# Kernel optimization log

Measured on AMD Instinct MI355X. Metric: run time of the kernel, lower is better.

## Reference

```python
import jax, jax.numpy as jnp
import numpy as np


def color_bin(x, n_bins):
    """Per-image 3D color histogram over n_bins**3 flat bins.
    x: [B, 3, H, W] float in ~[-1, 1]. Returns [B, n_bins**3] float32.
    """
    B, C, H, W = x.shape
    n_tot = n_bins ** 3
    # torch color_bins: i*(2/n_bins) - 1 for i in 1..n_bins-1
    boundaries = jnp.arange(1, n_bins, dtype=jnp.float32) * (2.0 / n_bins) - 1.0
    # torch.bucketize(right=False) == searchsorted side='left'
    idx = jnp.searchsorted(boundaries, x.reshape(B, C, H * W), side='left')  # [B,3,HW] int
    scale = jnp.array([1, n_bins, n_bins ** 2], dtype=idx.dtype)
    flat = jnp.einsum('bcp,c->bp', idx, scale)  # [B, HW], values in [0, n_tot)
    # torch.histc(bins, n_tot, min=0, max=n_tot-1) on exact integers == bincount
    hist = jax.vmap(lambda f: jnp.bincount(f, length=n_tot))(flat)
    return hist.astype(jnp.float32) / (H * W)


def setup_inputs() -> dict:
    key = jax.random.key(0)
    k1, k2 = jax.random.split(key)
    inp = jax.random.normal(k1, (8, 3, 1024, 1024), dtype=jnp.float32)
    style = jax.random.normal(k2, (1, 3, 1024, 1024), dtype=jnp.float32)
    return {"input": inp, "style_image": style, "n_bins": 16}


def reference(input, style_image, n_bins):
    # target histogram from the style image (detached in torch; ints anyway)
    target = color_bin(style_image, n_bins).squeeze(0)  # [n_tot]
    cols = color_bin(input, n_bins)                     # [B, n_tot]
    # F.l1_loss(cols, target.repeat(B, 1)) with mean reduction
    loss = jnp.mean(jnp.abs(cols - target[None, :]))
    return loss
```

## Files before the change

kernel.cpp:

```cpp
#include <hip/hip_runtime.h>

#define HW      (1024 * 1024)
#define HW4     (HW / 4)
#define NBINS   4096
#define NIMG    9
#define BPI     128
#define THREADS 256
#define F4_PER_BLOCK (HW4 / BPI)

__device__ __forceinline__ int bin16(float x) {
    int lo = 0;
    if (0.0f < x) lo = 8;
    if ((float)(lo + 4) * 0.125f - 1.0f < x) lo += 4;
    if ((float)(lo + 2) * 0.125f - 1.0f < x) lo += 2;
    if ((float)(lo + 1) * 0.125f - 1.0f < x) lo += 1;
    return lo;
}

__device__ __forceinline__ int bin3(float r, float g, float b) {
    return bin16(r) + 16 * bin16(g) + 256 * bin16(b);
}

__device__ __forceinline__ void acc4(int* lh, float4 r, float4 g, float4 b) {
    atomicAdd(&lh[bin3(r.x, g.x, b.x)], 1);
    atomicAdd(&lh[bin3(r.y, g.y, b.y)], 1);
    atomicAdd(&lh[bin3(r.z, g.z, b.z)], 1);
    atomicAdd(&lh[bin3(r.w, g.w, b.w)], 1);
}

__global__ __launch_bounds__(THREADS) void hist_kernel(
        const float* __restrict__ input,
        const float* __restrict__ style,
        int* __restrict__ part) {
    __shared__ int lh[NBINS];
    const int img = blockIdx.y;
    const int blk = blockIdx.x;
    const float* base = (img < 8) ? (input + (size_t)img * 3 * HW) : style;

    for (int i = threadIdx.x; i < NBINS; i += THREADS) lh[i] = 0;
    __syncthreads();

    const float4* c0 = (const float4*)(base);
    const float4* c1 = (const float4*)(base + HW);
    const float4* c2 = (const float4*)(base + 2 * HW);
    const int start = blk * F4_PER_BLOCK;

    for (int j = threadIdx.x; j < F4_PER_BLOCK; j += 2 * THREADS) {
        const int p0 = start + j;
        const int p1 = p0 + THREADS;
        float4 r0 = c0[p0], g0 = c1[p0], b0 = c2[p0];
        float4 r1 = c0[p1], g1 = c1[p1], b1 = c2[p1];
        acc4(lh, r0, g0, b0);
        acc4(lh, r1, g1, b1);
    }
    __syncthreads();

    int4* dst = (int4*)(part + ((size_t)img * BPI + blk) * NBINS);
    const int4* src = (const int4*)lh;
    for (int i = threadIdx.x; i < NBINS / 4; i += THREADS) dst[i] = src[i];
}

__global__ __launch_bounds__(THREADS) void reduce_kernel(
        const int* __restrict__ part,
        int* __restrict__ H) {
    const int img = blockIdx.y;
    const int bin = blockIdx.x * THREADS + threadIdx.x;
    const int* p = part + (size_t)img * BPI * NBINS + bin;
    int sum = 0;
#pragma unroll 8
    for (int b = 0; b < BPI; ++b) sum += p[(size_t)b * NBINS];
    H[img * NBINS + bin] = sum;
}

__global__ __launch_bounds__(1024) void loss_kernel(
        const int* __restrict__ H, float* __restrict__ out) {
    __shared__ long long partsum[16];
    const int* tgt = H + 8 * NBINS;
    long long acc = 0;
    for (int e = threadIdx.x; e < 8 * NBINS; e += 1024) {
        const int b = e >> 12;
        const int i = e & (NBINS - 1);
        const int d = H[b * NBINS + i] - tgt[i];
        acc += (d < 0) ? (long long)(-d) : (long long)d;
    }
    for (int off = 32; off; off >>= 1) acc += __shfl_down(acc, off, 64);
    const int lane = threadIdx.x & 63;
    const int wv   = threadIdx.x >> 6;
    if (lane == 0) partsum[wv] = acc;
    __syncthreads();
    if (wv == 0) {
        long long t = (lane < 16) ? partsum[lane] : 0;
        for (int off = 8; off; off >>= 1) t += __shfl_down(t, off, 64);
        if (lane == 0) {
            out[0] = (float)((double)t / 34359738368.0);
        }
    }
}

extern "C" void kernel_launch(void* const* d_in, const int* in_sizes, int n_in,
                              void* d_out, int out_size, void* d_ws, size_t ws_size,
                              hipStream_t stream) {
    const float* input = (const float*)d_in[0];
    const float* style = (const float*)d_in[1];
    int* part = (int*)d_ws;
    int* H    = part + (size_t)NIMG * BPI * NBINS;

    hipLaunchKernelGGL(hist_kernel, dim3(BPI, NIMG), dim3(THREADS), 0, stream,
                       input, style, part);
    hipLaunchKernelGGL(reduce_kernel, dim3(NBINS / THREADS, NIMG), dim3(THREADS),
                       0, stream, part, H);
    hipLaunchKernelGGL(loss_kernel, dim3(1), dim3(1024), 0, stream,
                       H, (float*)d_out);
}
```

Measured before the change: 182.1 us.

## Pack partial histograms to 16-bit, double blocks per image, split reduction

Doubles the number of histogram blocks per image so more workgroups run at once. Each block now handles 4096 pixels, so its bin counts fit in 16 bits and are written packed as ushort, which halves partial-histogram traffic. The reduction is split into two halves along a new grid dimension, and the loss kernel sums the two halves, stages the target histogram in shared memory, and accumulates in 32-bit ints instead of 64-bit. A bin count of exactly 65536 (all pixels of a block in one bin) would overflow the 16-bit packing.

After: 179.9 us. About the same (-1.2%).

```diff
diff --git a/kernel.cpp b/kernel.cpp
--- a/kernel.cpp
+++ b/kernel.cpp
@@ -4,9 +4,12 @@
 #define HW4     (HW / 4)
 #define NBINS   4096
 #define NIMG    9
-#define BPI     128
+#define BPI     256
 #define THREADS 256
 #define F4_PER_BLOCK (HW4 / BPI)
+#define NPART   (NIMG * BPI)
+
+typedef float f4 __attribute__((ext_vector_type(4)));
 
 __device__ __forceinline__ int bin16(float x) {
     int lo = 0;
@@ -21,7 +24,7 @@
     return bin16(r) + 16 * bin16(g) + 256 * bin16(b);
 }
 
-__device__ __forceinline__ void acc4(int* lh, float4 r, float4 g, float4 b) {
+__device__ __forceinline__ void acc4(int* lh, f4 r, f4 g, f4 b) {
     atomicAdd(&lh[bin3(r.x, g.x, b.x)], 1);
     atomicAdd(&lh[bin3(r.y, g.y, b.y)], 1);
     atomicAdd(&lh[bin3(r.z, g.z, b.z)], 1);
@@ -31,7 +34,7 @@
 __global__ __launch_bounds__(THREADS) void hist_kernel(
         const float* __restrict__ input,
         const float* __restrict__ style,
-        int* __restrict__ part) {
+        unsigned int* __restrict__ part) {
     __shared__ int lh[NBINS];
     const int img = blockIdx.y;
     const int blk = blockIdx.x;
@@ -40,48 +43,59 @@
     for (int i = threadIdx.x; i < NBINS; i += THREADS) lh[i] = 0;
     __syncthreads();
 
-    const float4* c0 = (const float4*)(base);
-    const float4* c1 = (const float4*)(base + HW);
-    const float4* c2 = (const float4*)(base + 2 * HW);
+    const f4* c0 = (const f4*)(base);
+    const f4* c1 = (const f4*)(base + HW);
+    const f4* c2 = (const f4*)(base + 2 * HW);
     const int start = blk * F4_PER_BLOCK;
 
     for (int j = threadIdx.x; j < F4_PER_BLOCK; j += 2 * THREADS) {
         const int p0 = start + j;
         const int p1 = p0 + THREADS;
-        float4 r0 = c0[p0], g0 = c1[p0], b0 = c2[p0];
-        float4 r1 = c0[p1], g1 = c1[p1], b1 = c2[p1];
+        f4 r0 = c0[p0], g0 = c1[p0], b0 = c2[p0];
+        f4 r1 = c0[p1], g1 = c1[p1], b1 = c2[p1];
         acc4(lh, r0, g0, b0);
         acc4(lh, r1, g1, b1);
     }
     __syncthreads();
 
-    int4* dst = (int4*)(part + ((size_t)img * BPI + blk) * NBINS);
-    const int4* src = (const int4*)lh;
-    for (int i = threadIdx.x; i < NBINS / 4; i += THREADS) dst[i] = src[i];
+    uint2* dst = (uint2*)(part + ((size_t)img * BPI + blk) * (NBINS / 2));
+    for (int i = threadIdx.x; i < NBINS / 4; i += THREADS) {
+        uint2 v;
+        v.x = (unsigned)lh[4 * i]     | ((unsigned)lh[4 * i + 1] << 16);
+        v.y = (unsigned)lh[4 * i + 2] | ((unsigned)lh[4 * i + 3] << 16);
+        dst[i] = v;
+    }
 }
 
 __global__ __launch_bounds__(THREADS) void reduce_kernel(
-        const int* __restrict__ part,
-        int* __restrict__ H) {
-    const int img = blockIdx.y;
-    const int bin = blockIdx.x * THREADS + threadIdx.x;
-    const int* p = part + (size_t)img * BPI * NBINS + bin;
+        const unsigned short* __restrict__ part,
+        int* __restrict__ H2) {
+    const int img  = blockIdx.y;
+    const int half = blockIdx.z;
+    const int bin  = blockIdx.x * THREADS + threadIdx.x;
+    const unsigned short* p = part
+        + ((size_t)img * BPI + half * (BPI / 2)) * NBINS + bin;
     int sum = 0;
-#pragma unroll 8
-    for (int b = 0; b < BPI; ++b) sum += p[(size_t)b * NBINS];
-    H[img * NBINS + bin] = sum;
+#pragma unroll 16
+    for (int b = 0; b < BPI / 2; ++b) sum += p[(size_t)b * NBINS];
+    H2[((size_t)half * NIMG + img) * NBINS + bin] = sum;
 }
 
 __global__ __launch_bounds__(1024) void loss_kernel(
-        const int* __restrict__ H, float* __restrict__ out) {
-    __shared__ long long partsum[16];
-    const int* tgt = H + 8 * NBINS;
-    long long acc = 0;
+        const int* __restrict__ H2, float* __restrict__ out) {
+    __shared__ int tgt_l[NBINS];
+    __shared__ int partsum[16];
+    const int* h0 = H2;
+    const int* h1 = H2 + NIMG * NBINS;
+    for (int i = threadIdx.x; i < NBINS; i += 1024)
+        tgt_l[i] = h0[8 * NBINS + i] + h1[8 * NBINS + i];
+    __syncthreads();
+
+    int acc = 0;
     for (int e = threadIdx.x; e < 8 * NBINS; e += 1024) {
-        const int b = e >> 12;
-        const int i = e & (NBINS - 1);
-        const int d = H[b * NBINS + i] - tgt[i];
-        acc += (d < 0) ? (long long)(-d) : (long long)d;
+        const int c = h0[e] + h1[e];
+        const int d = c - tgt_l[e & (NBINS - 1)];
+        acc += (d < 0) ? -d : d;
     }
     for (int off = 32; off; off >>= 1) acc += __shfl_down(acc, off, 64);
     const int lane = threadIdx.x & 63;
@@ -89,10 +103,10 @@
     if (lane == 0) partsum[wv] = acc;
     __syncthreads();
     if (wv == 0) {
-        long long t = (lane < 16) ? partsum[lane] : 0;
+        int t = (lane < 16) ? partsum[lane] : 0;
         for (int off = 8; off; off >>= 1) t += __shfl_down(t, off, 64);
         if (lane == 0) {
-            out[0] = (float)((double)t / 34359738368.0);
+            out[0] = (float)((double)(long long)t / 34359738368.0);
         }
     }
 }
@@ -102,13 +116,14 @@
                               hipStream_t stream) {
     const float* input = (const float*)d_in[0];
     const float* style = (const float*)d_in[1];
-    int* part = (int*)d_ws;
-    int* H    = part + (size_t)NIMG * BPI * NBINS;
+    unsigned int* part = (unsigned int*)d_ws;
+    int* H2 = (int*)((char*)d_ws + (size_t)NPART * NBINS * sizeof(unsigned short));
 
     hipLaunchKernelGGL(hist_kernel, dim3(BPI, NIMG), dim3(THREADS), 0, stream,
                        input, style, part);
-    hipLaunchKernelGGL(reduce_kernel, dim3(NBINS / THREADS, NIMG), dim3(THREADS),
-                       0, stream, part, H);
+    hipLaunchKernelGGL(reduce_kernel, dim3(NBINS / THREADS, NIMG, 2),
+                       dim3(THREADS), 0, stream,
+                       (const unsigned short*)part, H2);
     hipLaunchKernelGGL(loss_kernel, dim3(1), dim3(1024), 0, stream,
-                       H, (float*)d_out);
+                       H2, (float*)d_out);
 }
```
